# Performance work log

Measured on AMD Instinct MI355X. Metric: run time of the kernel, lower is better.

Reference implementation:

```python
import jax, jax.numpy as jnp
import numpy as np


def setup_inputs() -> dict:
    key = jax.random.key(0)
    ks = jax.random.split(key, 12)
    B, C, H, W = 8, 256, 64, 64
    inter = C // 8
    s = 0.05  # weight scale keeps q.k logits in a stable softmax range
    f32 = jnp.float32
    x = jax.random.normal(ks[0], (B, C, H, W), f32)
    Wq = jax.random.normal(ks[1], (inter, C), f32) * s
    bq = jnp.zeros((inter,), f32)
    Wk = jax.random.normal(ks[2], (inter, C), f32) * s
    bk = jnp.zeros((inter,), f32)
    Wv = jax.random.normal(ks[3], (C, C), f32) * s
    bv = jnp.zeros((C,), f32)
    gamma = jnp.full((1,), 0.5, f32)  # learnable residual scale (init 0 in torch; 0.5 exercises the path)
    Wg1 = jax.random.normal(ks[4], (inter, C), f32) * s
    bg1 = jnp.zeros((inter,), f32)
    Wg2 = jax.random.normal(ks[5], (C, inter), f32) * s
    bg2 = jnp.zeros((C,), f32)
    return {"x": x, "Wq": Wq, "bq": bq, "Wk": Wk, "bk": bk, "Wv": Wv, "bv": bv,
            "gamma": gamma, "Wg1": Wg1, "bg1": bg1, "Wg2": Wg2, "bg2": bg2}


def reference(x, Wq, bq, Wk, bk, Wv, bv, gamma, Wg1, bg1, Wg2, bg2):
    B, C, H, W = x.shape
    N = H * W
    xf = x.reshape(B, C, N)  # [B,C,N]
    # 1x1 convs == per-pixel linear projections
    q = jnp.einsum('oc,bcn->bon', Wq, xf) + bq[None, :, None]  # [B,inter,N]
    k = jnp.einsum('oc,bcn->bon', Wk, xf) + bk[None, :, None]  # [B,inter,N]
    v = jnp.einsum('oc,bcn->bon', Wv, xf) + bv[None, :, None]  # [B,C,N]
    # attention[b,n,m] = softmax_m( q[b,:,n] . k[b,:,m] )
    attn = jax.nn.softmax(jnp.einsum('bin,bim->bnm', q, k), axis=-1)  # [B,N,N]
    # out[b,c,n] = sum_m v[b,c,m] * attn[b,n,m]
    out = jnp.einsum('bcm,bnm->bcn', v, attn)  # [B,C,N]
    out = gamma[0] * out + xf
    # gated global pooling branch: GAP -> 1x1 conv -> ReLU -> 1x1 conv -> Sigmoid
    gp = xf.mean(axis=-1)  # [B,C]
    h = jax.nn.relu(jnp.einsum('oc,bc->bo', Wg1, gp) + bg1)  # [B,inter]
    ga = jax.nn.sigmoid(jnp.einsum('co,bo->bc', Wg2, h) + bg2)  # [B,C]
    out = out * ga[:, :, None] + out
    return out.reshape(B, C, H, W)
```

## Files before the change

kernel.cpp:

```cpp
#include <hip/hip_runtime.h>

typedef unsigned short u16;
typedef unsigned int   u32;
typedef short s16x4 __attribute__((ext_vector_type(4)));
typedef u16 u16x4 __attribute__((ext_vector_type(4)));
typedef u16 u16x8 __attribute__((ext_vector_type(8)));
typedef __bf16 bf16x8 __attribute__((ext_vector_type(8)));
typedef float f32x4 __attribute__((ext_vector_type(4)));
typedef float f32x2 __attribute__((ext_vector_type(2)));
typedef u32 u32x2v __attribute__((ext_vector_type(2)));
typedef u32 u32x4v __attribute__((ext_vector_type(4)));

#define NB 8
#define NC 256
#define NI 32
#define NN 4096
#define LOG2E 1.4426950408889634f
#define POFF 64.0f

#define OW_Q   0
#define OB_Q   8192
#define OW_K   8224
#define OB_K   16416
#define OW_V   16448
#define OB_V   81984
#define OGAM   82240
#define OW_G1  82248
#define OB_G1  90440
#define OW_G2  90472
#define OB_G2  98664
#define WTOT   98920

__device__ __forceinline__ float bf2f(u16 v) {
    u32 u = ((u32)v) << 16;
    return __builtin_bit_cast(float, u);
}
__device__ __forceinline__ u16 f2bf(float f) {
    u32 u = __builtin_bit_cast(u32, f);
    u32 lsb = (u >> 16) & 1u;
    u += 0x7fffu + lsb;
    return (u16)(u >> 16);
}
__device__ __forceinline__ u32 cvtpk_bf16(float lo, float hi) {
    u32 r;
    asm("v_cvt_pk_bf16_f32 %0, %1, %2" : "=v"(r) : "v"(lo), "v"(hi));
    return r;
}
__device__ __forceinline__ u16 f2bf_hw(float f) {
    u32 r;
    asm("v_cvt_pk_bf16_f32 %0, %1, %1" : "=v"(r) : "v"(f));
    return (u16)r;
}
__device__ __forceinline__ void permswap32(u32& a, u32& b) {
#if __has_builtin(__builtin_amdgcn_permlane32_swap)
    auto r = __builtin_amdgcn_permlane32_swap(a, b, false, false);
    a = (u32)r[0]; b = (u32)r[1];
#else
    int ln = (int)(threadIdx.x & 63);
    u32 a2 = (u32)__shfl_xor((int)a, 32, 64);
    u32 b2 = (u32)__shfl_xor((int)b, 32, 64);
    u32 na = (ln < 32) ? a : b2;
    u32 nb = (ln < 32) ? a2 : b;
    a = na; b = nb;
#endif
}
__device__ __forceinline__ void permswap16(u32& a, u32& b) {
#if __has_builtin(__builtin_amdgcn_permlane16_swap)
    auto r = __builtin_amdgcn_permlane16_swap(a, b, false, false);
    a = (u32)r[0]; b = (u32)r[1];
#else
    int q = (int)((threadIdx.x >> 4) & 1);
    u32 az = (u32)__shfl_xor((int)a, 16, 64);
    u32 bz = (u32)__shfl_xor((int)b, 16, 64);
    u32 na = q ? bz : a;
    u32 nb = q ? b  : az;
    a = na; b = nb;
#endif
}
__device__ __forceinline__ bool is_f32_mode(const void* graw) {
    return ((const u16*)graw)[0] == 0;
}

__global__ __launch_bounds__(256) void convert_kernel(
    const void* x,  const void* Wq, const void* bq, const void* Wk, const void* bk,
    const void* Wv, const void* bv, const void* gamma, const void* Wg1, const void* bg1,
    const void* Wg2, const void* bg2, float* __restrict__ xf, float* __restrict__ wbuf,
    u16* __restrict__ wbf, float* __restrict__ gp)
{
    bool f32m = is_f32_mode(gamma);
    int blk = blockIdx.x, t = threadIdx.x;
    if (blk < 2048) {
        int base = blk * 4096 + t * 16;
        float s = 0.f;
        if (f32m) {
            const float* xs = (const float*)x;
#pragma unroll
            for (int k = 0; k < 4; ++k) {
                f32x4 a = *(const f32x4*)(xs + base + k * 4);
                s += (a[0] + a[1]) + (a[2] + a[3]);
            }
        } else {
            const u16* xs = (const u16*)x;
#pragma unroll
            for (int k = 0; k < 2; ++k) {
                u16x8 a = *(const u16x8*)(xs + base + k * 8);
                f32x4 lo, hi;
#pragma unroll
                for (int j = 0; j < 4; ++j) { lo[j] = bf2f(a[j]); hi[j] = bf2f(a[4 + j]); }
                *(f32x4*)(xf + base + k * 8)     = lo;
                *(f32x4*)(xf + base + k * 8 + 4) = hi;
                s += (lo[0]+lo[1])+(lo[2]+lo[3]) + (hi[0]+hi[1])+(hi[2]+hi[3]);
            }
        }
#pragma unroll
        for (int off = 1; off <= 32; off <<= 1) s += __shfl_xor(s, off, 64);
        __shared__ float ws[4];
        if ((t & 63) == 0) ws[t >> 6] = s;
        __syncthreads();
        if (t == 0) gp[blk] = (ws[0] + ws[1] + ws[2] + ws[3]) * (1.0f / NN);
        return;
    }
    if (blk < 2080) {
        int tid = (blk - 2048) * 256 + t;
        const int off[12] = {OW_Q, OB_Q, OW_K, OB_K, OW_V, OB_V, OGAM, OW_G1, OB_G1, OW_G2, OB_G2, WTOT};
        const int len[11] = {8192, 32, 8192, 32, 65536, 256, 1, 8192, 32, 8192, 256};
        const void* srcs[11] = {Wq, bq, Wk, bk, Wv, bv, gamma, Wg1, bg1, Wg2, bg2};
        for (int w = tid; w < WTOT; w += 32 * 256) {
            int seg = 0;
#pragma unroll
            for (int i = 1; i < 11; ++i) if (w >= off[i]) seg = i;
            int idx = w - off[seg];
            float val = 0.f;
            if (idx < len[seg])
                val = f32m ? ((const float*)srcs[seg])[idx] : bf2f(((const u16*)srcs[seg])[idx]);
            wbuf[w] = val;
        }
        return;
    }
    int tid = (blk - 2080) * 256 + t;
    for (int w = tid; w < 320 * 256; w += 10 * 256) {
        int row = w >> 8, c = w & 255;
        const void* src; int idx; float scale = 1.f;
        if (row < 32)      { src = Wq; idx = row * 256 + c; scale = LOG2E; }
        else if (row < 64) { src = Wk; idx = (row - 32) * 256 + c; }
        else               { src = Wv; idx = (row - 64) * 256 + c; }
        float val = f32m ? ((const float*)src)[idx] : bf2f(((const u16*)src)[idx]);
        wbf[w] = f2bf(val * scale);
    }
}

__global__ __launch_bounds__(256) void proj_kernel(
    const void* xr, const float* __restrict__ xf, const void* graw,
    const float* __restrict__ wbuf, const u16* __restrict__ wbf,
    u16* __restrict__ qt, u16* __restrict__ kt, u16* __restrict__ v)
{
    __shared__ __attribute__((aligned(16))) u16 xs[64][264];

    const float* X = is_f32_mode(graw) ? (const float*)xr : xf;

    int t    = threadIdx.x;
    int lane = t & 63;
    int wave = t >> 6;
    int b    = blockIdx.x >> 6;
    int m0   = (blockIdx.x & 63) << 6;
    int l15  = lane & 15;
    int quad = lane >> 4;

    {
        const float* xb = X + (size_t)b * NC * NN + m0 + lane;
        int c0 = wave * 64;
#pragma unroll
        for (int ci = 0; ci < 64; ci += 4) {
            int c = c0 + ci;
            float a0 = xb[(size_t)(c    ) * NN];
            float a1 = xb[(size_t)(c + 1) * NN];
            float a2 = xb[(size_t)(c + 2) * NN];
            float a3 = xb[(size_t)(c + 3) * NN];
            u32x2v p2;
            p2.x = cvtpk_bf16(a0, a1);
            p2.y = cvtpk_bf16(a2, a3);
            *(u32x2v*)&xs[lane][c] = p2;
        }
    }
    __syncthreads();

    const f32x4 zero4 = {};
    f32x4 acc[5][4];
#pragma unroll
    for (int i = 0; i < 5; ++i)
#pragma unroll
        for (int mt = 0; mt < 4; ++mt) acc[i][mt] = zero4;

    int obase = wave * 80;
    const u16* wb = wbf + (size_t)(obase + l15) * 256 + quad * 8;

    bf16x8 af[5];
#pragma unroll
    for (int i = 0; i < 5; ++i)
        af[i] = *(const bf16x8*)(wb + (size_t)(i * 16) * 256);

#pragma unroll
    for (int kc = 0; kc < 8; ++kc) {
        bf16x8 afn[5], bfr[4];
        if (kc < 7) {
#pragma unroll
            for (int i = 0; i < 5; ++i)
                afn[i] = *(const bf16x8*)(wb + (size_t)(i * 16) * 256 + (kc + 1) * 32);
        }
#pragma unroll
        for (int mt = 0; mt < 4; ++mt)
            bfr[mt] = *(const bf16x8*)&xs[mt * 16 + l15][kc * 32 + quad * 8];
#pragma unroll
        for (int i = 0; i < 5; ++i)
#pragma unroll
            for (int mt = 0; mt < 4; ++mt)
                acc[i][mt] = __builtin_amdgcn_mfma_f32_16x16x32_bf16(af[i], bfr[mt], acc[i][mt], 0, 0, 0);
        if (kc < 7) {
#pragma unroll
            for (int i = 0; i < 5; ++i) af[i] = afn[i];
        }
    }

    __syncthreads();

    if (wave == 0) {
#pragma unroll
        for (int i = 0; i < 4; ++i) {
#pragma unroll
            for (int mt = 0; mt < 4; ++mt) {
                float tv[4];
#pragma unroll
                for (int r = 0; r < 4; ++r) {
                    int o = i * 16 + quad * 4 + r;
                    float bias = (o < 32) ? LOG2E * wbuf[OB_Q + o] : wbuf[OB_K + o - 32];
                    tv[r] = acc[i][mt][r] + bias;
                }
                u32x2v p2;
                p2.x = cvtpk_bf16(tv[0], tv[1]);
                p2.y = cvtpk_bf16(tv[2], tv[3]);
                *(u32x2v*)&xs[mt * 16 + l15][i * 16 + quad * 4] = p2;
            }
        }
        int m = m0 + lane;
        u16* qrow = qt + (size_t)(b * NN + m) * NI;
        u16* krow = kt + (size_t)(b * NN + m) * NI;
#pragma unroll
        for (int j = 0; j < 4; ++j) *(u16x8*)(qrow + j * 8) = *(const u16x8*)&xs[lane][j * 8];
#pragma unroll
        for (int j = 0; j < 4; ++j) *(u16x8*)(krow + j * 8) = *(const u16x8*)&xs[lane][32 + j * 8];
#pragma unroll
        for (int mt = 0; mt < 4; ++mt) {
#pragma unroll
            for (int r = 0; r < 4; ++r) {
                int c = quad * 4 + r;
                v[(size_t)(b * NC + c) * NN + m0 + mt * 16 + l15] = f2bf_hw(acc[4][mt][r] + wbuf[OB_V + c]);
            }
        }
    } else {
#pragma unroll
        for (int i = 0; i < 5; ++i) {
#pragma unroll
            for (int mt = 0; mt < 4; ++mt) {
#pragma unroll
                for (int r = 0; r < 4; ++r) {
                    int c = wave * 80 + i * 16 + quad * 4 + r - 64;
                    v[(size_t)(b * NC + c) * NN + m0 + mt * 16 + l15] = f2bf_hw(acc[i][mt][r] + wbuf[OB_V + c]);
                }
            }
        }
    }
}

__global__ __launch_bounds__(256) void gate_kernel(
    const float* __restrict__ gp, const float* __restrict__ wbuf, float* __restrict__ gmul)
{
    int b = blockIdx.x;
    int t = threadIdx.x;
    __shared__ float gps[NC];
    __shared__ float hs[NI];
    gps[t] = gp[b * NC + t];
    __syncthreads();
    if (t < NI) {
        float a = wbuf[OB_G1 + t];
        for (int c = 0; c < NC; ++c) a += wbuf[OW_G1 + t * NC + c] * gps[c];
        hs[t] = a > 0.f ? a : 0.f;
    }
    __syncthreads();
    float a = wbuf[OB_G2 + t];
#pragma unroll
    for (int i = 0; i < NI; ++i) a += wbuf[OW_G2 + t * NI + i] * hs[i];
    float sig = 1.f / (1.f + __expf(-a));
    gmul[b * NC + t] = 1.f + sig;
}

__global__ __launch_bounds__(512, 4) void flash_kernel(
    const u16* __restrict__ qt, const u16* __restrict__ kt, const u16* __restrict__ v,
    const void* xr, const float* __restrict__ xf, const void* graw,
    const float* __restrict__ wbuf, const float* __restrict__ gmul, void* outp)
{
    __shared__ __attribute__((aligned(16))) u16 vs[2][NC][40];

    bool f32m = is_f32_mode(graw);
    const float* X = f32m ? (const float*)xr : xf;

    int t    = threadIdx.x;
    int lane = t & 63;
    int wave = t >> 6;
    int b    = blockIdx.x & 7;
    int nblk = (blockIdx.x >> 3) << 6;
    int n0   = nblk + (wave >> 2) * 32;
    int c0   = (wave & 3) * 64;
    int l15  = lane & 15;
    int quad = lane >> 4;

    const f32x4 zero4 = {};
    const f32x4 mneg  = {-POFF, -POFF, -POFF, -POFF};

    bf16x8 qf[2];
#pragma unroll
    for (int n16 = 0; n16 < 2; ++n16)
        qf[n16] = *(const bf16x8*)(qt + (size_t)(b * NN + n0 + n16 * 16 + l15) * NI + quad * 8);

    f32x4 acc[2][4];
#pragma unroll
    for (int n16 = 0; n16 < 2; ++n16)
#pragma unroll
        for (int ct = 0; ct < 4; ++ct) acc[n16][ct] = zero4;
    f32x2 psum2[2] = {};

    int sc = t >> 2;
    int sm = (t & 3) * 8;
    const u16* vb0 = v + (size_t)(b * NC + sc) * NN + sm;
    const u16* vb1 = v + (size_t)(b * NC + sc + 128) * NN + sm;
    const u16* ktb = kt + (size_t)(b * NN + l15) * NI + quad * 8;

    u16x8 vr0 = *(const u16x8*)vb0;
    u16x8 vr1 = *(const u16x8*)vb1;
    *(u16x8*)&vs[0][sc][sm]       = vr0;
    *(u16x8*)&vs[0][sc + 128][sm] = vr1;
    bf16x8 ktf[2];
#pragma unroll
    for (int mt = 0; mt < 2; ++mt)
        ktf[mt] = *(const bf16x8*)(ktb + (size_t)(mt * 16) * NI);
    __syncthreads();

    for (int it = 0; it < NN / 32; ++it) {
        int cur  = it & 1;
        bool more = (it < NN / 32 - 1);
        int mnxt = it * 32 + 32;

        if (more) {
            vr0 = *(const u16x8*)(vb0 + mnxt);
            vr1 = *(const u16x8*)(vb1 + mnxt);
        }

        f32x4 sf[2][2];
#pragma unroll
        for (int mt = 0; mt < 2; ++mt)
#pragma unroll
            for (int n16 = 0; n16 < 2; ++n16)
                sf[n16][mt] = __builtin_amdgcn_mfma_f32_16x16x32_bf16(ktf[mt], qf[n16], mneg, 0, 0, 0);

        bf16x8 va8[4];
#pragma unroll
        for (int ct = 0; ct < 4; ++ct)
            va8[ct] = *(const bf16x8*)&vs[cur][c0 + ct * 16 + l15][quad * 8];

        if (more) {
#pragma unroll
            for (int mt = 0; mt < 2; ++mt)
                ktf[mt] = *(const bf16x8*)(ktb + (size_t)(mnxt + mt * 16) * NI);
        }

        bf16x8 pfr8[2];
#pragma unroll
        for (int n16 = 0; n16 < 2; ++n16) {
            float p[2][4];
#pragma unroll
            for (int mt = 0; mt < 2; ++mt)
#pragma unroll
                for (int r = 0; r < 4; ++r)
                    p[mt][r] = __builtin_amdgcn_exp2f(sf[n16][mt][r]);
            f32x2 t0; t0.x = p[0][0]; t0.y = p[0][1];
            f32x2 t1; t1.x = p[0][2]; t1.y = p[0][3];
            f32x2 t2; t2.x = p[1][0]; t2.y = p[1][1];
            f32x2 t3; t3.x = p[1][2]; t3.y = p[1][3];
            psum2[n16] += (t0 + t1) + (t2 + t3);
            u32 A0 = cvtpk_bf16(p[0][0], p[0][1]);
            u32 A1 = cvtpk_bf16(p[0][2], p[0][3]);
            u32 B0 = cvtpk_bf16(p[1][0], p[1][1]);
            u32 B1 = cvtpk_bf16(p[1][2], p[1][3]);
            permswap32(A0, B0); permswap16(A0, B0);
            permswap32(A1, B1); permswap16(A1, B1);
            u32x4v f; f.x = A0; f.y = A1; f.z = B0; f.w = B1;
            pfr8[n16] = __builtin_bit_cast(bf16x8, f);
        }

#pragma unroll
        for (int ct = 0; ct < 4; ++ct)
#pragma unroll
            for (int n16 = 0; n16 < 2; ++n16)
                acc[n16][ct] = __builtin_amdgcn_mfma_f32_16x16x32_bf16(va8[ct], pfr8[n16], acc[n16][ct], 0, 0, 0);

        if (more) {
            *(u16x8*)&vs[cur ^ 1][sc][sm]       = vr0;
            *(u16x8*)&vs[cur ^ 1][sc + 128][sm] = vr1;
        }
        __syncthreads();
    }

    float inv[2];
#pragma unroll
    for (int n16 = 0; n16 < 2; ++n16) {
        float s = psum2[n16].x + psum2[n16].y;
        s += __shfl_xor(s, 16, 64);
        s += __shfl_xor(s, 32, 64);
        inv[n16] = 1.f / s;
    }
    float gam = wbuf[OGAM];

#pragma unroll
    for (int n16 = 0; n16 < 2; ++n16) {
        int n = n0 + n16 * 16 + l15;
#pragma unroll
        for (int ct = 0; ct < 4; ++ct) {
            int cb = c0 + ct * 16 + quad * 4;
            f32x4 gm4 = *(const f32x4*)&gmul[b * NC + cb];
#pragma unroll
            for (int r = 0; r < 4; ++r) {
                size_t off = (size_t)(b * NC + cb + r) * NN + n;
                float val = (gam * acc[n16][ct][r] * inv[n16] + X[off]) * gm4[r];
                if (f32m) ((float*)outp)[off] = val;
                else      ((u16*)outp)[off]  = f2bf_hw(val);
            }
        }
    }
}

extern "C" void kernel_launch(void* const* d_in, const int* in_sizes, int n_in,
                              void* d_out, int out_size, void* d_ws, size_t ws_size,
                              hipStream_t stream)
{
    const void* x     = d_in[0];
    const void* Wq    = d_in[1];
    const void* bq    = d_in[2];
    const void* Wk    = d_in[3];
    const void* bk    = d_in[4];
    const void* Wv    = d_in[5];
    const void* bvp   = d_in[6];
    const void* gamma = d_in[7];
    const void* Wg1   = d_in[8];
    const void* bg1   = d_in[9];
    const void* Wg2   = d_in[10];
    const void* bg2   = d_in[11];

    char* ws = (char*)d_ws;
    float* xf   = (float*)ws;
    float* wbuf = (float*)(ws + 33554432);
    u16*   qt   = (u16*)  (ws + 33951744);
    u16*   kt   = (u16*)  (ws + 36048896);
    u16*   v    = (u16*)  (ws + 38146048);
    float* gp   = (float*)(ws + 54923264);
    float* gmul = (float*)(ws + 54931456);
    u16*   wbf  = (u16*)  (ws + 54939648);

    convert_kernel<<<2090, 256, 0, stream>>>(x, Wq, bq, Wk, bk, Wv, bvp, gamma,
                                             Wg1, bg1, Wg2, bg2, xf, wbuf, wbf, gp);
    proj_kernel<<<NB * 64, 256, 0, stream>>>(x, xf, gamma, wbuf, wbf, qt, kt, v);
    gate_kernel<<<NB, 256, 0, stream>>>(gp, wbuf, gmul);
    flash_kernel<<<NB * 64, 512, 0, stream>>>(qt, kt, v, x, xf, gamma, wbuf, gmul, d_out);
}
```

Measured before the change: 280.6 us.

## Double V tile to 64 keys per stage with two-deep register prefetch

```diff
diff --git a/kernel.cpp b/kernel.cpp
--- a/kernel.cpp
+++ b/kernel.cpp
@@ -298,7 +298,7 @@
     const void* xr, const float* __restrict__ xf, const void* graw,
     const float* __restrict__ wbuf, const float* __restrict__ gmul, void* outp)
 {
-    __shared__ __attribute__((aligned(16))) u16 vs[2][NC][40];
+    __shared__ __attribute__((aligned(16))) u16 vs[2][2][NC][40];
 
     bool f32m = is_f32_mode(graw);
     const float* X = f32m ? (const float*)xr : xf;
@@ -313,8 +313,7 @@
     int l15  = lane & 15;
     int quad = lane >> 4;
 
-    const f32x4 zero4 = {};
-    const f32x4 mneg  = {-POFF, -POFF, -POFF, -POFF};
+    const f32x4 mneg = {-POFF, -POFF, -POFF, -POFF};
 
     bf16x8 qf[2];
 #pragma unroll
@@ -325,7 +324,7 @@
 #pragma unroll
     for (int n16 = 0; n16 < 2; ++n16)
 #pragma unroll
-        for (int ct = 0; ct < 4; ++ct) acc[n16][ct] = zero4;
+        for (int ct = 0; ct < 4; ++ct) acc[n16][ct] = f32x4{};
     f32x2 psum2[2] = {};
 
     int sc = t >> 2;
@@ -334,78 +333,94 @@
     const u16* vb1 = v + (size_t)(b * NC + sc + 128) * NN + sm;
     const u16* ktb = kt + (size_t)(b * NN + l15) * NI + quad * 8;
 
-    u16x8 vr0 = *(const u16x8*)vb0;
-    u16x8 vr1 = *(const u16x8*)vb1;
-    *(u16x8*)&vs[0][sc][sm]       = vr0;
-    *(u16x8*)&vs[0][sc + 128][sm] = vr1;
-    bf16x8 ktf[2];
-#pragma unroll
-    for (int mt = 0; mt < 2; ++mt)
-        ktf[mt] = *(const bf16x8*)(ktb + (size_t)(mt * 16) * NI);
+    u16x8 sr0, sr1, sr2, sr3;
+    sr0 = *(const u16x8*)(vb0);        sr1 = *(const u16x8*)(vb1);
+    sr2 = *(const u16x8*)(vb0 + 32);   sr3 = *(const u16x8*)(vb1 + 32);
+    *(u16x8*)&vs[0][0][sc][sm]       = sr0;
+    *(u16x8*)&vs[0][0][sc + 128][sm] = sr1;
+    *(u16x8*)&vs[0][1][sc][sm]       = sr2;
+    *(u16x8*)&vs[0][1][sc + 128][sm] = sr3;
+    sr0 = *(const u16x8*)(vb0 + 64);   sr1 = *(const u16x8*)(vb1 + 64);
+    sr2 = *(const u16x8*)(vb0 + 96);   sr3 = *(const u16x8*)(vb1 + 96);
+    bf16x8 ktA[2], ktB[2];
+    ktA[0] = *(const bf16x8*)(ktb);
+    ktA[1] = *(const bf16x8*)(ktb + (size_t)16 * NI);
+    ktB[0] = *(const bf16x8*)(ktb + (size_t)32 * NI);
+    ktB[1] = *(const bf16x8*)(ktb + (size_t)48 * NI);
     __syncthreads();
 
-    for (int it = 0; it < NN / 32; ++it) {
-        int cur  = it & 1;
-        bool more = (it < NN / 32 - 1);
-        int mnxt = it * 32 + 32;
-
-        if (more) {
-            vr0 = *(const u16x8*)(vb0 + mnxt);
-            vr1 = *(const u16x8*)(vb1 + mnxt);
-        }
-
-        f32x4 sf[2][2];
-#pragma unroll
-        for (int mt = 0; mt < 2; ++mt)
-#pragma unroll
-            for (int n16 = 0; n16 < 2; ++n16)
-                sf[n16][mt] = __builtin_amdgcn_mfma_f32_16x16x32_bf16(ktf[mt], qf[n16], mneg, 0, 0, 0);
-
-        bf16x8 va8[4];
-#pragma unroll
-        for (int ct = 0; ct < 4; ++ct)
-            va8[ct] = *(const bf16x8*)&vs[cur][c0 + ct * 16 + l15][quad * 8];
-
-        if (more) {
+    for (int it = 0; it < 64; ++it) {
+        int p = it & 1;
+        bool wmore = (it < 63);
+        bool lmore = (it < 62);
+
+        if (wmore) {
+            *(u16x8*)&vs[p ^ 1][0][sc][sm]       = sr0;
+            *(u16x8*)&vs[p ^ 1][0][sc + 128][sm] = sr1;
+            *(u16x8*)&vs[p ^ 1][1][sc][sm]       = sr2;
+            *(u16x8*)&vs[p ^ 1][1][sc + 128][sm] = sr3;
+        }
+        if (lmore) {
+            int cb = it * 64 + 128;
+            sr0 = *(const u16x8*)(vb0 + cb);
+            sr1 = *(const u16x8*)(vb1 + cb);
+            sr2 = *(const u16x8*)(vb0 + cb + 32);
+            sr3 = *(const u16x8*)(vb1 + cb + 32);
+        }
+
+#pragma unroll
+        for (int h = 0; h < 2; ++h) {
+            bf16x8* ktX = (h == 0) ? ktA : ktB;
+
+            f32x4 sf[2][2];
 #pragma unroll
             for (int mt = 0; mt < 2; ++mt)
-                ktf[mt] = *(const bf16x8*)(ktb + (size_t)(mnxt + mt * 16) * NI);
-        }
-
-        bf16x8 pfr8[2];
-#pragma unroll
-        for (int n16 = 0; n16 < 2; ++n16) {
-            float p[2][4];
-#pragma unroll
-            for (int mt = 0; mt < 2; ++mt)
-#pragma unroll
-                for (int r = 0; r < 4; ++r)
-                    p[mt][r] = __builtin_amdgcn_exp2f(sf[n16][mt][r]);
-            f32x2 t0; t0.x = p[0][0]; t0.y = p[0][1];
-            f32x2 t1; t1.x = p[0][2]; t1.y = p[0][3];
-            f32x2 t2; t2.x = p[1][0]; t2.y = p[1][1];
-            f32x2 t3; t3.x = p[1][2]; t3.y = p[1][3];
-            psum2[n16] += (t0 + t1) + (t2 + t3);
-            u32 A0 = cvtpk_bf16(p[0][0], p[0][1]);
-            u32 A1 = cvtpk_bf16(p[0][2], p[0][3]);
-            u32 B0 = cvtpk_bf16(p[1][0], p[1][1]);
-            u32 B1 = cvtpk_bf16(p[1][2], p[1][3]);
-            permswap32(A0, B0); permswap16(A0, B0);
-            permswap32(A1, B1); permswap16(A1, B1);
-            u32x4v f; f.x = A0; f.y = A1; f.z = B0; f.w = B1;
-            pfr8[n16] = __builtin_bit_cast(bf16x8, f);
-        }
-
-#pragma unroll
-        for (int ct = 0; ct < 4; ++ct)
-#pragma unroll
-            for (int n16 = 0; n16 < 2; ++n16)
-                acc[n16][ct] = __builtin_amdgcn_mfma_f32_16x16x32_bf16(va8[ct], pfr8[n16], acc[n16][ct], 0, 0, 0);
-
-        if (more) {
-            *(u16x8*)&vs[cur ^ 1][sc][sm]       = vr0;
-            *(u16x8*)&vs[cur ^ 1][sc + 128][sm] = vr1;
-        }
+#pragma unroll
+                for (int n16 = 0; n16 < 2; ++n16)
+                    sf[n16][mt] = __builtin_amdgcn_mfma_f32_16x16x32_bf16(ktX[mt], qf[n16], mneg, 0, 0, 0);
+
+            bf16x8 va8[4];
+#pragma unroll
+            for (int ct = 0; ct < 4; ++ct)
+                va8[ct] = *(const bf16x8*)&vs[p][h][c0 + ct * 16 + l15][quad * 8];
+
+            if (wmore) {
+                int mg = it * 64 + 64 + h * 32;
+                ktX[0] = *(const bf16x8*)(ktb + (size_t)mg * NI);
+                ktX[1] = *(const bf16x8*)(ktb + (size_t)(mg + 16) * NI);
+            }
+
+            bf16x8 pfr8[2];
+#pragma unroll
+            for (int n16 = 0; n16 < 2; ++n16) {
+                float pp[2][4];
+#pragma unroll
+                for (int mt = 0; mt < 2; ++mt)
+#pragma unroll
+                    for (int r = 0; r < 4; ++r)
+                        pp[mt][r] = __builtin_amdgcn_exp2f(sf[n16][mt][r]);
+                f32x2 t0; t0.x = pp[0][0]; t0.y = pp[0][1];
+                f32x2 t1; t1.x = pp[0][2]; t1.y = pp[0][3];
+                f32x2 t2; t2.x = pp[1][0]; t2.y = pp[1][1];
+                f32x2 t3; t3.x = pp[1][2]; t3.y = pp[1][3];
+                psum2[n16] += (t0 + t1) + (t2 + t3);
+                u32 A0 = cvtpk_bf16(pp[0][0], pp[0][1]);
+                u32 A1 = cvtpk_bf16(pp[0][2], pp[0][3]);
+                u32 B0 = cvtpk_bf16(pp[1][0], pp[1][1]);
+                u32 B1 = cvtpk_bf16(pp[1][2], pp[1][3]);
+                permswap32(A0, B0); permswap16(A0, B0);
+                permswap32(A1, B1); permswap16(A1, B1);
+                u32x4v f; f.x = A0; f.y = A1; f.z = B0; f.w = B1;
+                pfr8[n16] = __builtin_bit_cast(bf16x8, f);
+            }
+
+#pragma unroll
+            for (int ct = 0; ct < 4; ++ct)
+#pragma unroll
+                for (int n16 = 0; n16 < 2; ++n16)
+                    acc[n16][ct] = __builtin_amdgcn_mfma_f32_16x16x32_bf16(va8[ct], pfr8[n16], acc[n16][ct], 0, 0, 0);
+        }
+
         __syncthreads();
     }
 
```

Result: faster. 270.0 us (-3.8%).
